# Kernel optimization log

Measured on AMD Instinct MI355X. Metric: run time of the kernel, lower is better.

The kernel has to match this reference:

```python
import jax, jax.numpy as jnp
import numpy as np

B, S, D = 2, 8192, 1024
H, DK, DV = 8, 64, 64
DH = 4096
SEG = 2048
NSEG = S // SEG
EPS = 1e-5


def setup_inputs() -> dict:
    key = jax.random.key(0)
    ks = jax.random.split(key, 9)
    g = lambda k, shp, sc: jax.random.normal(k, shp, jnp.float32) * sc
    return {
        "x": g(ks[0], (B, S, D), 1.0),
        "Wq": g(ks[1], (D, H * DK), 0.02),
        "Wk": g(ks[2], (D, H * DK), 0.02),
        "Wv": g(ks[3], (D, H * DV), 0.02),
        "Wo": g(ks[4], (H * DV, D), 0.02),
        "betas": g(ks[5], (1, H, 1, DV), 1.0),
        "W1": g(ks[6], (D, DH), 0.02),
        "b1": jnp.zeros((DH,), jnp.float32),
        "W2": g(ks[7], (DH, D), 0.02),
        "b2": jnp.zeros((D,), jnp.float32),
        "ln_g": jnp.ones((D,), jnp.float32),
        "ln_b": jnp.zeros((D,), jnp.float32),
    }


def _compressive_memory(x, Wq, Wk, Wv, Wo, betas):
    # project and split heads: (B, H, S, d)
    q = (x @ Wq).reshape(B, S, H, DK).transpose(0, 2, 1, 3)
    k = (x @ Wk).reshape(B, S, H, DK).transpose(0, 2, 1, 3)
    v = (x @ Wv).reshape(B, S, H, DV).transpose(0, 2, 1, 3)

    # chunk into segments: (NSEG, B, H, SEG, d)
    seg = lambda t, d: t.reshape(B, H, NSEG, SEG, d).transpose(2, 0, 1, 3, 4)
    qs, ks_, vs = seg(q, DK), seg(k, DK), seg(v, DV)

    mem0 = jnp.zeros((B, H, DK, DV), jnp.float32)
    z0 = jnp.ones((B, H, DK, 1), jnp.float32) / DK
    causal_mask = jnp.tril(jnp.ones((SEG, SEG), bool))
    scale = np.float32(1.0 / np.sqrt(DK))
    gate = jax.nn.sigmoid(betas)  # (1, H, 1, DV)

    def step(carry, inp):
        mem, z = carry
        qi, ki, vi = inp  # (B, H, SEG, d)
        sq = jax.nn.elu(qi) + 1.0
        sk = jax.nn.elu(ki) + 1.0
        # memory retrieval (uses state from previous segments)
        att_mem = (sq @ mem) / (sq @ z)  # (B, H, SEG, DV)
        # local causal SDP attention within the segment
        scores = jnp.einsum('bhqd,bhkd->bhqk', qi, ki) * scale
        scores = jnp.where(causal_mask, scores, -jnp.inf)
        att_dot = jax.nn.softmax(scores, axis=-1) @ vi
        # linear memory update
        mem = mem + jnp.einsum('bhsd,bhsv->bhdv', sk, vi)
        z = z + sk.sum(axis=-2, keepdims=True).transpose(0, 1, 3, 2)
        att = gate * att_mem + (1.0 - gate) * att_dot
        return (mem, z), att

    _, atts = jax.lax.scan(step, (mem0, z0), (qs, ks_, vs))
    # (NSEG, B, H, SEG, DV) -> (B, S, H*DV)
    att = atts.transpose(1, 0, 3, 2, 4).reshape(B, S, H * DV)
    return att @ Wo


def reference(x, Wq, Wk, Wv, Wo, betas, W1, b1, W2, b2, ln_g, ln_b):
    a = _compressive_memory(x, Wq, Wk, Wv, Wo, betas)
    h = jax.nn.gelu(a @ W1 + b1, approximate=False) @ W2 + b2
    y = h + x
    mu = y.mean(axis=-1, keepdims=True)
    var = ((y - mu) ** 2).mean(axis=-1, keepdims=True)
    return (y - mu) / jnp.sqrt(var + EPS) * ln_g + ln_b
```

## Files before the change

kernel.cpp:

```cpp
#include <hip/hip_runtime.h>
#include <hip/hip_bf16.h>
#include <math.h>

#define B_    2
#define S_    8192
#define D_    1024
#define H_N   8
#define DK_   64
#define DV_   64
#define DH_   4096
#define SEG_  2048
#define NSEG_ 4
#define EPS_  1e-5f
#define LDQKV 1536

typedef __hip_bfloat16 bf16;
typedef unsigned int u32;
typedef __attribute__((ext_vector_type(8))) short bf16x8;
typedef __attribute__((ext_vector_type(4))) float f32x4;

union bvec { bf16x8 v; bf16 e[8]; };

template <typename T> __device__ inline T from_f(float v);
template <> __device__ inline float from_f<float>(float v) { return v; }
template <> __device__ inline bf16  from_f<bf16>(float v)  { return __float2bfloat16(v); }

__device__ __forceinline__ void gld_lds16(const bf16* g, bf16* l) {
    __builtin_amdgcn_global_load_lds(
        (const __attribute__((address_space(1))) u32*)g,
        (__attribute__((address_space(3))) u32*)l, 16, 0, 0);
}

__device__ inline float elu1(float x) { return x > 0.f ? x + 1.f : __expf(x); }

#define GP(APTR, BPTR, MH, LOADB)                                              \
    {                                                                          \
        if (LOADB) {                                                           \
            _Pragma("unroll")                                                  \
            for (int n = 0; n < 4; n++)                                        \
                bg[n] = *(const bf16x8*)((BPTR) + n * 2048);                   \
        }                                                                      \
        _Pragma("unroll")                                                      \
        for (int m = 0; m < 4; m++)                                            \
            af[m] = *(const bf16x8*)((APTR) + (MH) * 8192 + m * 2048);         \
        asm volatile("s_waitcnt lgkmcnt(0)" ::: "memory");                     \
        __builtin_amdgcn_sched_barrier(0);                                     \
        __builtin_amdgcn_s_setprio(1);                                         \
        _Pragma("unroll")                                                      \
        for (int m = 0; m < 4; m++)                                            \
            _Pragma("unroll")                                                  \
            for (int n = 0; n < 4; n++)                                        \
                acc[(MH) * 4 + m][n] = __builtin_amdgcn_mfma_f32_16x16x32_bf16(\
                    af[m], bg[n], acc[(MH) * 4 + m][n], 0, 0, 0);              \
        __builtin_amdgcn_s_setprio(0);                                         \
    }

template <int EPI, typename CT>
__global__ __launch_bounds__(512, 1) void gemm256(
    const bf16* __restrict__ A, const bf16* __restrict__ BT, CT* __restrict__ C,
    const float* __restrict__ bias, const float* __restrict__ resid,
    int M, int N, int K)
{
    __shared__ bf16 L0[32768];
    __shared__ bf16 L1[32768];
    const int t    = threadIdx.x;
    const int lane = t & 63;
    const int w    = t >> 6;
    const int la   = lane & 15;
    const int g    = lane >> 4;

    const int nx  = gridDim.x;
    const int nwg = nx * gridDim.y;
    const int lin = blockIdx.y * nx + blockIdx.x;
    const int swzb = (lin & 7) * (nwg >> 3) + (lin >> 3);
    const int by  = swzb / nx, bx = swzb - by * nx;

    const int m0 = by * 256, n0 = bx * 256;
    const int wm = w >> 2, wn = w & 3;

    f32x4 acc[8][4];
    #pragma unroll
    for (int m = 0; m < 8; m++)
        #pragma unroll
        for (int n = 0; n < 4; n++) {
            f32x4 z4 = {0.f, 0.f, 0.f, 0.f};
            acc[m][n] = z4;
        }

    const int nt = K >> 6;

    const int rq = w * 8 + (lane >> 3);
    const int c8 = ((lane & 7) ^ (lane >> 3)) * 8;
    auto stageQ = [&](int kt_, int q, bf16* Lb) {
        const size_t k0 = (size_t)kt_ << 6;
        gld_lds16(A  + (size_t)(m0 + q * 64 + rq) * K + k0 + c8,
                  Lb + q * 4096 + w * 512);
        gld_lds16(BT + (size_t)(n0 + q * 64 + rq) * K + k0 + c8,
                  Lb + 16384 + q * 4096 + w * 512);
    };

    const int sw0 = (g ^ (la & 7)) << 4;
    const int sw1 = ((4 + g) ^ (la & 7)) << 4;
    const int aoff = (wm * 128 + la) * 128;
    const int boff = 32768 + (wn * 64 + la) * 128;
    const char* a0k0 = (const char*)L0 + aoff + sw0;
    const char* a0k1 = (const char*)L0 + aoff + sw1;
    const char* b0k0 = (const char*)L0 + boff + sw0;
    const char* b0k1 = (const char*)L0 + boff + sw1;
    const char* a1k0 = (const char*)L1 + aoff + sw0;
    const char* a1k1 = (const char*)L1 + aoff + sw1;
    const char* b1k0 = (const char*)L1 + boff + sw0;
    const char* b1k1 = (const char*)L1 + boff + sw1;

    stageQ(0, 0, L0); stageQ(0, 1, L0); stageQ(0, 2, L0); stageQ(0, 3, L0);

    bf16x8 af[4], bg[4];
    for (int tt = 0; tt < nt; tt += 2) {
        const bool more = (tt + 2 < nt);
        __builtin_amdgcn_s_barrier();
        stageQ(tt + 1, 0, L1);
        asm volatile("s_waitcnt vmcnt(2)" ::: "memory");
        __builtin_amdgcn_sched_barrier(0);
        __builtin_amdgcn_s_barrier();
        GP(a0k0, b0k0, 0, true);
        __builtin_amdgcn_s_barrier();
        stageQ(tt + 1, 1, L1);
        GP(a0k0, b0k0, 1, false);
        __builtin_amdgcn_s_barrier();
        stageQ(tt + 1, 2, L1);
        GP(a0k1, b0k1, 0, true);
        __builtin_amdgcn_s_barrier();
        stageQ(tt + 1, 3, L1);
        GP(a0k1, b0k1, 1, false);
        __builtin_amdgcn_s_barrier();
        if (more) {
            stageQ(tt + 2, 0, L0);
            asm volatile("s_waitcnt vmcnt(2)" ::: "memory");
        } else {
            asm volatile("s_waitcnt vmcnt(0)" ::: "memory");
        }
        __builtin_amdgcn_sched_barrier(0);
        __builtin_amdgcn_s_barrier();
        GP(a1k0, b1k0, 0, true);
        __builtin_amdgcn_s_barrier();
        if (more) stageQ(tt + 2, 1, L0);
        GP(a1k0, b1k0, 1, false);
        __builtin_amdgcn_s_barrier();
        if (more) stageQ(tt + 2, 2, L0);
        GP(a1k1, b1k1, 0, true);
        __builtin_amdgcn_s_barrier();
        if (more) stageQ(tt + 2, 3, L0);
        GP(a1k1, b1k1, 1, false);
    }

    const int row0 = m0 + wm * 128 + g * 4;
    const int col0 = n0 + wn * 64 + la;
    float bj[4];
    if (EPI >= 2) {
        #pragma unroll
        for (int n = 0; n < 4; n++) bj[n] = bias[col0 + n * 16];
    }
    #pragma unroll
    for (int m = 0; m < 8; m++) {
        #pragma unroll
        for (int r = 0; r < 4; r++) {
            const int row = row0 + m * 16 + r;
            #pragma unroll
            for (int n = 0; n < 4; n++) {
                const int col = col0 + n * 16;
                float v = acc[m][n][r];
                if (EPI >= 2) v += bj[n];
                if (EPI == 2) v = 0.5f * v * (1.0f + erff(v * 0.70710678118654752f));
                if (EPI == 3) v += resid[(size_t)row * N + col];
                C[(size_t)row * N + col] = from_f<CT>(v);
            }
        }
    }
}

__global__ __launch_bounds__(256) void castx_k(const float* __restrict__ X,
                                               bf16* __restrict__ Y)
{
    size_t i = ((size_t)blockIdx.x * 256 + threadIdx.x) * 4;
    float4 v = *(const float4*)(X + i);
    union { bf16 b[4]; unsigned long long u; } o;
    o.b[0] = __float2bfloat16(v.x);
    o.b[1] = __float2bfloat16(v.y);
    o.b[2] = __float2bfloat16(v.z);
    o.b[3] = __float2bfloat16(v.w);
    *(unsigned long long*)(Y + i) = o.u;
}

__global__ __launch_bounds__(256) void transcast_k(const float* __restrict__ W,
                                                   bf16* __restrict__ WT, int K, int N)
{
    __shared__ float tile[32][33];
    const int n0 = blockIdx.x * 32, k0 = blockIdx.y * 32;
    const int tx = threadIdx.x & 31, ty = threadIdx.x >> 5;
    #pragma unroll
    for (int i = 0; i < 32; i += 8)
        tile[ty + i][tx] = W[(size_t)(k0 + ty + i) * N + n0 + tx];
    __syncthreads();
    #pragma unroll
    for (int i = 0; i < 32; i += 8)
        WT[(size_t)(n0 + ty + i) * K + k0 + tx] = __float2bfloat16(tile[tx][ty + i]);
}

__global__ __launch_bounds__(256) void vtrans_k(const bf16* __restrict__ V,
                                                bf16* __restrict__ Vt)
{
    __shared__ bf16 t_[64 * 64];
    const int t = threadIdx.x;
    const int sblk = blockIdx.x & 127;
    const int b = blockIdx.x >> 7;
    const int h = blockIdx.y;
    const bf16* src = V + ((size_t)b * S_ + sblk * 64) * LDQKV + h * 64;
    #pragma unroll
    for (int k = 0; k < 2; k++) {
        int e = t + k * 256;
        int r = e >> 3, c8 = (e & 7) * 8;
        *(bf16x8*)&t_[r * 64 + c8] = *(const bf16x8*)&src[(size_t)r * LDQKV + c8];
    }
    __syncthreads();
    const int dv = t & 63, s0 = (t >> 6) * 16;
    bf16* dst = Vt + ((size_t)(b * 8 + h) * 64 + dv) * (size_t)S_ + sblk * 64 + s0;
    bvec o0, o1;
    #pragma unroll
    for (int i = 0; i < 8; i++) {
        o0.e[i] = t_[(s0 + i) * 64 + dv];
        o1.e[i] = t_[(s0 + 8 + i) * 64 + dv];
    }
    *(bf16x8*)dst = o0.v;
    *(bf16x8*)(dst + 8) = o1.v;
}

__global__ __launch_bounds__(256) void memseg_k(
    const bf16* __restrict__ Kg, const bf16* __restrict__ Vg,
    float* __restrict__ MP, float* __restrict__ ZP)
{
    __shared__ float Ks[64][65];
    __shared__ float Vs[64][65];
    const int t = threadIdx.x, tx = t & 15, ty = t >> 4;
    const int sb = blockIdx.x;
    const int seg = sb >> 4, bh = sb & 15;
    const int b = bh >> 3, h = bh & 7;
    const int chunk = blockIdx.y;
    const size_t base = ((size_t)b * S_ + (size_t)seg * SEG_ + (size_t)chunk * 512) * LDQKV + h * 64;

    float acc[4][4] = {};
    float zacc[4]   = {};
    for (int st = 0; st < 8; st++) {
        #pragma unroll
        for (int kk = 0; kk < 2; kk++) {
            int e = t + kk * 256;
            int r = e >> 3, c8 = (e & 7) * 8;
            size_t go = base + ((size_t)st * 64 + r) * LDQKV + c8;
            bvec kv_, vv_;
            kv_.v = *(const bf16x8*)&Kg[go];
            vv_.v = *(const bf16x8*)&Vg[go];
            #pragma unroll
            for (int i = 0; i < 8; i++) {
                Ks[r][c8 + i] = elu1(__bfloat162float(kv_.e[i]));
                Vs[r][c8 + i] = __bfloat162float(vv_.e[i]);
            }
        }
        __syncthreads();
        for (int s = 0; s < 64; s++) {
            float a4[4], v4[4];
            #pragma unroll
            for (int i = 0; i < 4; i++) a4[i] = Ks[s][ty * 4 + i];
            #pragma unroll
            for (int j = 0; j < 4; j++) v4[j] = Vs[s][tx * 4 + j];
            #pragma unroll
            for (int i = 0; i < 4; i++)
                #pragma unroll
                for (int j = 0; j < 4; j++)
                    acc[i][j] += a4[i] * v4[j];
        }
        #pragma unroll
        for (int ii = 0; ii < 4; ii++) {
            int s = tx + ii * 16;
            #pragma unroll
            for (int i = 0; i < 4; i++) zacc[i] += Ks[s][ty * 4 + i];
        }
        __syncthreads();
    }
    const int slot = (seg * 4 + chunk) * 16 + bh;
    #pragma unroll
    for (int i = 0; i < 4; i++)
        #pragma unroll
        for (int j = 0; j < 4; j++)
            MP[(size_t)slot * 4096 + (ty * 4 + i) * 64 + tx * 4 + j] = acc[i][j];
    #pragma unroll
    for (int i = 0; i < 4; i++) {
        float zz = zacc[i];
        #pragma unroll
        for (int mk = 1; mk < 16; mk <<= 1) zz += __shfl_xor(zz, mk);
        if (tx == 0) ZP[slot * 64 + ty * 4 + i] = zz;
    }
}

__global__ __launch_bounds__(256) void prefix_k(
    const float* __restrict__ MP, const float* __restrict__ ZP,
    bf16* __restrict__ MST, float* __restrict__ ZS)
{
    const int bh = blockIdx.x, t = threadIdx.x;
    for (int e = t; e < 4096; e += 256) {
        int dk = e >> 6, dv = e & 63;
        float s = 0.f;
        #pragma unroll
        for (int slot = 0; slot < 16; slot++) {
            if ((slot & 3) == 0)
                MST[(size_t)((slot >> 2) * 16 + bh) * 4096 + dv * 64 + dk] = __float2bfloat16(s);
            s += MP[(size_t)(slot * 16 + bh) * 4096 + e];
        }
    }
    if (t < 64) {
        float s = 1.0f / DK_;
        #pragma unroll
        for (int slot = 0; slot < 16; slot++) {
            if ((slot & 3) == 0) ZS[((slot >> 2) * 16 + bh) * 64 + t] = s;
            s += ZP[(slot * 16 + bh) * 64 + t];
        }
    }
}

template <int NG>
__device__ __forceinline__ void stageT(const bf16* gsrc, size_t stride, bf16* lds,
                                       int wave, int lane)
{
    #pragma unroll
    for (int ii = 0; ii < NG; ii++) {
        int i = wave * NG + ii;
        gld_lds16(gsrc + (size_t)(8 * i + (lane >> 3)) * stride
                        + (size_t)(((lane & 7) ^ (lane >> 3)) * 8),
                  lds + i * 512);
    }
}

__device__ __forceinline__ bf16x8 ldsw128(const bf16* base, int row, int colE)
{
    int off = row * 128 + ((colE * 2) ^ ((row & 7) << 4));
    return *(const bf16x8*)((const char*)base + off);
}

__global__ __launch_bounds__(256) void attn_k(
    const bf16* __restrict__ Qg, const bf16* __restrict__ Kg, const bf16* __restrict__ Vt,
    const bf16* __restrict__ MsT, const float* __restrict__ ZS,
    const float* __restrict__ betas, bf16* __restrict__ att)
{
    __shared__ bf16 KT[2][4096];
    __shared__ bf16 VTs[2][4096];
    __shared__ bf16 QP[8192];
    __shared__ float Zsm[64];

    const int t    = threadIdx.x;
    const int lane = t & 63;
    const int w    = t >> 6;
    const int la   = lane & 15;
    const int g    = lane >> 4;
    const int qt   = (int)gridDim.x - 1 - (int)blockIdx.x;
    const int bh   = blockIdx.y;
    const int seg  = blockIdx.z;
    const int b    = bh >> 3, h = bh & 7;

    const size_t srow = (size_t)b * S_ + (size_t)seg * SEG_;
    const bf16* qp  = Qg + (srow + (size_t)qt * 128) * LDQKV + h * 64;
    const bf16* kp  = Kg + srow * LDQKV + h * 64;
    const bf16* vtp = Vt + (size_t)bh * 64 * (size_t)S_ + (size_t)seg * SEG_;

    stageT<4>(qp, LDQKV, QP, w, lane);
    stageT<2>(kp, LDQKV, KT[0], w, lane);
    stageT<2>(vtp, S_, VTs[0], w, lane);
    if (t < 64) Zsm[t] = ZS[(seg * 16 + bh) * 64 + t];
    __syncthreads();

    bf16x8 aq[2][2];
    #pragma unroll
    for (int st = 0; st < 2; st++)
        #pragma unroll
        for (int s = 0; s < 2; s++)
            aq[st][s] = ldsw128(QP, w * 32 + st * 16 + la, s * 32 + g * 8);

    float m_[2] = {-1e30f, -1e30f};
    float l_[2] = {0.f, 0.f};
    f32x4 Oa[2][4];
    #pragma unroll
    for (int st = 0; st < 2; st++)
        #pragma unroll
        for (int j = 0; j < 4; j++) { f32x4 z4 = {0.f,0.f,0.f,0.f}; Oa[st][j] = z4; }

    const int jtmax = 2 * qt + 1;
    int cur = 0;
    for (int jt = 0; jt <= jtmax; jt++, cur ^= 1) {
        if (jt < jtmax) {
            stageT<2>(kp + (size_t)(jt + 1) * 64 * LDQKV, LDQKV, KT[cur ^ 1], w, lane);
            stageT<2>(vtp + (size_t)(jt + 1) * 64, S_, VTs[cur ^ 1], w, lane);
        }

        bf16x8 kf[2][4];
        #pragma unroll
        for (int s = 0; s < 2; s++)
            #pragma unroll
            for (int j = 0; j < 4; j++)
                kf[s][j] = ldsw128(KT[cur], j * 16 + la, s * 32 + g * 8);

        const int jtkv = jt * 64;
        #pragma unroll
        for (int st = 0; st < 2; st++) {
            f32x4 sc[4];
            #pragma unroll
            for (int j = 0; j < 4; j++) { f32x4 z4 = {0.f,0.f,0.f,0.f}; sc[j] = z4; }
            #pragma unroll
            for (int j = 0; j < 4; j++) {
                sc[j] = __builtin_amdgcn_mfma_f32_16x16x32_bf16(kf[0][j], aq[st][0], sc[j], 0, 0, 0);
                sc[j] = __builtin_amdgcn_mfma_f32_16x16x32_bf16(kf[1][j], aq[st][1], sc[j], 0, 0, 0);
            }

            const int q_abs = qt * 128 + w * 32 + st * 16 + la;
            float sv[4][4];
            float mx = -1e30f;
            #pragma unroll
            for (int j = 0; j < 4; j++)
                #pragma unroll
                for (int r = 0; r < 4; r++) {
                    float v = sc[j][r] * 0.125f;
                    int kv = jtkv + j * 16 + g * 4 + r;
                    v = (kv <= q_abs) ? v : -1e30f;
                    sv[j][r] = v;
                    mx = fmaxf(mx, v);
                }
            mx = fmaxf(mx, __shfl_xor(mx, 16));
            mx = fmaxf(mx, __shfl_xor(mx, 32));
            float mnew = fmaxf(m_[st], mx);
            float corr = __expf(m_[st] - mnew);
            float rs = 0.f;
            #pragma unroll
            for (int j = 0; j < 4; j++)
                #pragma unroll
                for (int r = 0; r < 4; r++) {
                    float p = __expf(sv[j][r] - mnew);
                    sv[j][r] = p;
                    rs += p;
                }
            rs += __shfl_xor(rs, 16);
            rs += __shfl_xor(rs, 32);
            l_[st] = l_[st] * corr + rs;
            m_[st] = mnew;

            const int R = w * 32 + st * 16 + la;
            #pragma unroll
            for (int j = 0; j < 4; j++) {
                union { bf16 e[4]; uint2 u; } pk;
                #pragma unroll
                for (int r = 0; r < 4; r++) pk.e[r] = __float2bfloat16(sv[j][r]);
                int off = R * 128 + ((j * 32 + g * 8) ^ ((la & 7) << 4));
                *(uint2*)((char*)QP + off) = pk.u;
            }

            #pragma unroll
            for (int r = 0; r < 4; r++) {
                float corr_r = __shfl(corr, (lane & 48) | (g * 4 + r));
                #pragma unroll
                for (int j = 0; j < 4; j++) Oa[st][j][r] *= corr_r;
            }
        }

        asm volatile("s_waitcnt lgkmcnt(0)" ::: "memory");
        __builtin_amdgcn_sched_barrier(0);

        bf16x8 bv[2][4];
        #pragma unroll
        for (int s = 0; s < 2; s++)
            #pragma unroll
            for (int j = 0; j < 4; j++)
                bv[s][j] = ldsw128(VTs[cur], j * 16 + la, s * 32 + g * 8);
        #pragma unroll
        for (int st = 0; st < 2; st++) {
            bf16x8 ap0 = ldsw128(QP, w * 32 + st * 16 + la, g * 8);
            bf16x8 ap1 = ldsw128(QP, w * 32 + st * 16 + la, 32 + g * 8);
            #pragma unroll
            for (int j = 0; j < 4; j++) {
                Oa[st][j] = __builtin_amdgcn_mfma_f32_16x16x32_bf16(ap0, bv[0][j], Oa[st][j], 0, 0, 0);
                Oa[st][j] = __builtin_amdgcn_mfma_f32_16x16x32_bf16(ap1, bv[1][j], Oa[st][j], 0, 0, 0);
            }
        }
        __syncthreads();
    }

    stageT<2>(MsT + (size_t)(seg * 16 + bh) * 4096, 64, KT[0], w, lane);
    __syncthreads();

    bf16x8 sq[2][2];
    float den[2] = {0.f, 0.f};
    #pragma unroll
    for (int st = 0; st < 2; st++) {
        #pragma unroll
        for (int s = 0; s < 2; s++) {
            bvec in, outv;
            in.v = aq[st][s];
            #pragma unroll
            for (int e = 0; e < 8; e++) {
                float f = elu1(__bfloat162float(in.e[e]));
                outv.e[e] = __float2bfloat16(f);
                den[st] += f * Zsm[s * 32 + 8 * g + e];
            }
            sq[st][s] = outv.v;
        }
        den[st] += __shfl_xor(den[st], 16);
        den[st] += __shfl_xor(den[st], 32);
    }

    bf16x8 bm[2][4];
    #pragma unroll
    for (int s = 0; s < 2; s++)
        #pragma unroll
        for (int j = 0; j < 4; j++)
            bm[s][j] = ldsw128(KT[0], j * 16 + la, s * 32 + g * 8);

    float gate[4];
    #pragma unroll
    for (int j = 0; j < 4; j++)
        gate[j] = 1.f / (1.f + __expf(-betas[h * 64 + j * 16 + la]));

    #pragma unroll
    for (int st = 0; st < 2; st++) {
        f32x4 num[4];
        #pragma unroll
        for (int j = 0; j < 4; j++) { f32x4 z4 = {0.f,0.f,0.f,0.f}; num[j] = z4; }
        #pragma unroll
        for (int j = 0; j < 4; j++) {
            num[j] = __builtin_amdgcn_mfma_f32_16x16x32_bf16(sq[st][0], bm[0][j], num[j], 0, 0, 0);
            num[j] = __builtin_amdgcn_mfma_f32_16x16x32_bf16(sq[st][1], bm[1][j], num[j], 0, 0, 0);
        }
        #pragma unroll
        for (int r = 0; r < 4; r++) {
            float den_r = __shfl(den[st], (lane & 48) | (g * 4 + r));
            float l_r   = __shfl(l_[st],  (lane & 48) | (g * 4 + r));
            float linv  = 1.f / l_r;
            float dinv  = 1.f / den_r;
            size_t orow = srow + (size_t)qt * 128 + w * 32 + st * 16 + g * 4 + r;
            #pragma unroll
            for (int j = 0; j < 4; j++) {
                float am = num[j][r] * dinv;
                float ad = Oa[st][j][r] * linv;
                att[orow * 512 + h * 64 + j * 16 + la] =
                    __float2bfloat16(gate[j] * am + (1.f - gate[j]) * ad);
            }
        }
    }
}

__global__ __launch_bounds__(256) void ln_k(
    const float* __restrict__ Y, const float* __restrict__ g,
    const float* __restrict__ bta, float* __restrict__ out)
{
    const int row = blockIdx.x;
    const float* yp = Y + (size_t)row * D_;
    const int t = threadIdx.x;
    float v[4];
    float s = 0.f, s2 = 0.f;
    #pragma unroll
    for (int i = 0; i < 4; i++) {
        v[i] = yp[t + i * 256];
        s += v[i]; s2 += v[i] * v[i];
    }
    #pragma unroll
    for (int mk = 1; mk < 64; mk <<= 1) {
        s  += __shfl_xor(s, mk);
        s2 += __shfl_xor(s2, mk);
    }
    __shared__ float ss[4], ss2[4];
    int w = t >> 6;
    if ((t & 63) == 0) { ss[w] = s; ss2[w] = s2; }
    __syncthreads();
    s  = ss[0] + ss[1] + ss[2] + ss[3];
    s2 = ss2[0] + ss2[1] + ss2[2] + ss2[3];
    float mu   = s / D_;
    float var  = s2 / D_ - mu * mu;
    float rstd = rsqrtf(var + EPS_);
    #pragma unroll
    for (int i = 0; i < 4; i++) {
        int c = t + i * 256;
        out[(size_t)row * D_ + c] = (v[i] - mu) * rstd * g[c] + bta[c];
    }
}

extern "C" void kernel_launch(void* const* d_in, const int* in_sizes, int n_in,
                              void* d_out, int out_size, void* d_ws, size_t ws_size,
                              hipStream_t stream)
{
    const float* x     = (const float*)d_in[0];
    const float* Wq    = (const float*)d_in[1];
    const float* Wk    = (const float*)d_in[2];
    const float* Wv    = (const float*)d_in[3];
    const float* Wo    = (const float*)d_in[4];
    const float* betas = (const float*)d_in[5];
    const float* W1    = (const float*)d_in[6];
    const float* b1    = (const float*)d_in[7];
    const float* W2    = (const float*)d_in[8];
    const float* b2    = (const float*)d_in[9];
    const float* lng   = (const float*)d_in[10];
    const float* lnb   = (const float*)d_in[11];
    float* out = (float*)d_out;

    const int M = B_ * S_;
    char* base = (char*)d_ws;
    const size_t MB = 1024 * 1024;

    bf16*  Ab    = (bf16*)(base);
    bf16*  Hb    = (bf16*)(base + 32 * MB);
    bf16*  Xbf   = (bf16*)(base + 32 * MB);
    bf16*  QKV   = (bf16*)(base + 64 * MB);
    bf16*  Vt    = (bf16*)(base + 112 * MB);
    bf16*  ATT   = (bf16*)(base + 128 * MB);
    bf16*  WqkvT = (bf16*)(base + 160 * MB);
    bf16*  WoT   = (bf16*)(base + 163 * MB);
    bf16*  W1T   = (bf16*)(base + 164 * MB);
    bf16*  W2T   = (bf16*)(base + 172 * MB);
    float* MP    = (float*)(base + 180 * MB);
    bf16*  MST   = (bf16*)(base + 184 * MB);
    float* ZP    = (float*)(base + 185 * MB);
    float* ZS    = (float*)(base + 185 * MB + 256 * 1024);

    dim3 blk(256);
    dim3 blk512(512);

    castx_k<<<dim3((M * D_) / 1024), blk, 0, stream>>>(x, Xbf);
    transcast_k<<<dim3(512 / 32, 1024 / 32), blk, 0, stream>>>(Wq, WqkvT, 1024, 512);
    transcast_k<<<dim3(512 / 32, 1024 / 32), blk, 0, stream>>>(Wk, WqkvT + 512 * 1024, 1024, 512);
    transcast_k<<<dim3(512 / 32, 1024 / 32), blk, 0, stream>>>(Wv, WqkvT + 1024 * 1024, 1024, 512);
    transcast_k<<<dim3(1024 / 32, 512 / 32), blk, 0, stream>>>(Wo, WoT, 512, 1024);
    transcast_k<<<dim3(4096 / 32, 1024 / 32), blk, 0, stream>>>(W1, W1T, 1024, 4096);
    transcast_k<<<dim3(1024 / 32, 4096 / 32), blk, 0, stream>>>(W2, W2T, 4096, 1024);

    gemm256<0, bf16><<<dim3(1536 / 256, M / 256), blk512, 0, stream>>>(
        Xbf, WqkvT, QKV, nullptr, nullptr, M, 1536, 1024);

    vtrans_k<<<dim3(256, 8), blk, 0, stream>>>(QKV + 1024, Vt);

    memseg_k<<<dim3(NSEG_ * 16, 4), blk, 0, stream>>>(QKV + 512, QKV + 1024, MP, ZP);
    prefix_k<<<dim3(16), blk, 0, stream>>>(MP, ZP, MST, ZS);

    attn_k<<<dim3(SEG_ / 128, 16, NSEG_), blk, 0, stream>>>(
        QKV, QKV + 512, Vt, MST, ZS, betas, ATT);

    gemm256<0, bf16><<<dim3(1024 / 256, M / 256), blk512, 0, stream>>>(
        ATT, WoT, Ab, nullptr, nullptr, M, 1024, 512);
    gemm256<2, bf16><<<dim3(4096 / 256, M / 256), blk512, 0, stream>>>(
        Ab, W1T, Hb, b1, nullptr, M, 4096, 1024);
    gemm256<3, float><<<dim3(1024 / 256, M / 256), blk512, 0, stream>>>(
        Hb, W2T, out, b2, x, M, 1024, 4096);

    ln_k<<<dim3(M), blk, 0, stream>>>(out, lng, lnb, out);
}
```

Before: 699.7 us.

## Split memory-state partial sums finer and parallelize prefix scan; fuse QKV weight transposes

```diff
diff --git a/kernel.cpp b/kernel.cpp
--- a/kernel.cpp
+++ b/kernel.cpp
@@ -206,6 +206,24 @@
         WT[(size_t)(n0 + ty + i) * K + k0 + tx] = __float2bfloat16(tile[tx][ty + i]);
 }
 
+__global__ __launch_bounds__(256) void transqkv_k(
+    const float* __restrict__ Wq, const float* __restrict__ Wk,
+    const float* __restrict__ Wv, bf16* __restrict__ WT)
+{
+    __shared__ float tile[32][33];
+    const float* W = (blockIdx.z == 0) ? Wq : (blockIdx.z == 1) ? Wk : Wv;
+    bf16* dst = WT + (size_t)blockIdx.z * 512 * 1024;
+    const int n0 = blockIdx.x * 32, k0 = blockIdx.y * 32;
+    const int tx = threadIdx.x & 31, ty = threadIdx.x >> 5;
+    #pragma unroll
+    for (int i = 0; i < 32; i += 8)
+        tile[ty + i][tx] = W[(size_t)(k0 + ty + i) * 512 + n0 + tx];
+    __syncthreads();
+    #pragma unroll
+    for (int i = 0; i < 32; i += 8)
+        dst[(size_t)(n0 + ty + i) * 1024 + k0 + tx] = __float2bfloat16(tile[tx][ty + i]);
+}
+
 __global__ __launch_bounds__(256) void vtrans_k(const bf16* __restrict__ V,
                                                 bf16* __restrict__ Vt)
 {
@@ -245,11 +263,11 @@
     const int seg = sb >> 4, bh = sb & 15;
     const int b = bh >> 3, h = bh & 7;
     const int chunk = blockIdx.y;
-    const size_t base = ((size_t)b * S_ + (size_t)seg * SEG_ + (size_t)chunk * 512) * LDQKV + h * 64;
+    const size_t base = ((size_t)b * S_ + (size_t)seg * SEG_ + (size_t)chunk * 128) * LDQKV + h * 64;
 
     float acc[4][4] = {};
     float zacc[4]   = {};
-    for (int st = 0; st < 8; st++) {
+    for (int st = 0; st < 2; st++) {
         #pragma unroll
         for (int kk = 0; kk < 2; kk++) {
             int e = t + kk * 256;
@@ -285,7 +303,7 @@
         }
         __syncthreads();
     }
-    const int slot = (seg * 4 + chunk) * 16 + bh;
+    const int slot = (seg * 16 + chunk) * 16 + bh;
     #pragma unroll
     for (int i = 0; i < 4; i++)
         #pragma unroll
@@ -304,23 +322,21 @@
     const float* __restrict__ MP, const float* __restrict__ ZP,
     bf16* __restrict__ MST, float* __restrict__ ZS)
 {
-    const int bh = blockIdx.x, t = threadIdx.x;
-    for (int e = t; e < 4096; e += 256) {
-        int dk = e >> 6, dv = e & 63;
-        float s = 0.f;
-        #pragma unroll
-        for (int slot = 0; slot < 16; slot++) {
-            if ((slot & 3) == 0)
-                MST[(size_t)((slot >> 2) * 16 + bh) * 4096 + dv * 64 + dk] = __float2bfloat16(s);
-            s += MP[(size_t)(slot * 16 + bh) * 4096 + e];
-        }
-    }
-    if (t < 64) {
-        float s = 1.0f / DK_;
-        #pragma unroll
-        for (int slot = 0; slot < 16; slot++) {
-            if ((slot & 3) == 0) ZS[((slot >> 2) * 16 + bh) * 64 + t] = s;
-            s += ZP[(slot * 16 + bh) * 64 + t];
+    const int bh = blockIdx.x;
+    const int e  = blockIdx.y * 256 + threadIdx.x;
+    const int dk = e >> 6, dv = e & 63;
+    float s = 0.f;
+    for (int si = 0; si < 64; si++) {
+        if ((si & 15) == 0)
+            MST[(size_t)((si >> 4) * 16 + bh) * 4096 + dv * 64 + dk] = __float2bfloat16(s);
+        s += MP[(size_t)(si * 16 + bh) * 4096 + e];
+    }
+    if (blockIdx.y == 0 && threadIdx.x < 64) {
+        const int dz = threadIdx.x;
+        float z = 1.0f / DK_;
+        for (int si = 0; si < 64; si++) {
+            if ((si & 15) == 0) ZS[((si >> 4) * 16 + bh) * 64 + dz] = z;
+            z += ZP[(si * 16 + bh) * 64 + dz];
         }
     }
 }
@@ -619,17 +635,15 @@
     bf16*  W1T   = (bf16*)(base + 164 * MB);
     bf16*  W2T   = (bf16*)(base + 172 * MB);
     float* MP    = (float*)(base + 180 * MB);
-    bf16*  MST   = (bf16*)(base + 184 * MB);
-    float* ZP    = (float*)(base + 185 * MB);
-    float* ZS    = (float*)(base + 185 * MB + 256 * 1024);
+    bf16*  MST   = (bf16*)(base + 196 * MB);
+    float* ZP    = (float*)(base + 197 * MB);
+    float* ZS    = (float*)(base + 197 * MB + 512 * 1024);
 
     dim3 blk(256);
     dim3 blk512(512);
 
     castx_k<<<dim3((M * D_) / 1024), blk, 0, stream>>>(x, Xbf);
-    transcast_k<<<dim3(512 / 32, 1024 / 32), blk, 0, stream>>>(Wq, WqkvT, 1024, 512);
-    transcast_k<<<dim3(512 / 32, 1024 / 32), blk, 0, stream>>>(Wk, WqkvT + 512 * 1024, 1024, 512);
-    transcast_k<<<dim3(512 / 32, 1024 / 32), blk, 0, stream>>>(Wv, WqkvT + 1024 * 1024, 1024, 512);
+    transqkv_k<<<dim3(16, 32, 3), blk, 0, stream>>>(Wq, Wk, Wv, WqkvT);
     transcast_k<<<dim3(1024 / 32, 512 / 32), blk, 0, stream>>>(Wo, WoT, 512, 1024);
     transcast_k<<<dim3(4096 / 32, 1024 / 32), blk, 0, stream>>>(W1, W1T, 1024, 4096);
     transcast_k<<<dim3(1024 / 32, 4096 / 32), blk, 0, stream>>>(W2, W2T, 4096, 1024);
@@ -639,8 +653,8 @@
 
     vtrans_k<<<dim3(256, 8), blk, 0, stream>>>(QKV + 1024, Vt);
 
-    memseg_k<<<dim3(NSEG_ * 16, 4), blk, 0, stream>>>(QKV + 512, QKV + 1024, MP, ZP);
-    prefix_k<<<dim3(16), blk, 0, stream>>>(MP, ZP, MST, ZS);
+    memseg_k<<<dim3(NSEG_ * 16, 16), blk, 0, stream>>>(QKV + 512, QKV + 1024, MP, ZP);
+    prefix_k<<<dim3(16, 16), blk, 0, stream>>>(MP, ZP, MST, ZS);
 
     attn_k<<<dim3(SEG_ / 128, 16, NSEG_), blk, 0, stream>>>(
         QKV, QKV + 512, Vt, MST, ZS, betas, ATT);
```

After: 688.0 us. About the same (-1.7%).
